# Kernel tuning notes

Measured on AMD Instinct MI355X. Metric: run time of the kernel, lower is better.

## Reference

```python
import jax, jax.numpy as jnp
import numpy as np

NHEAD = 8; DM = 512; DFF = 2048; L = 4; S = 1024; NTOK = 51; MLP = 256; CLASSES = 7
GH = 3; GHID = 64; GCLS = 5; ALPHA = 0.2
HD = DM // NHEAD

_ADJ = np.array([[0,1,0,0,0],[1,1,1,1,0],[1,0,1,0,1],[1,0,0,1,1],[0,0,1,1,1]], dtype=np.int32)


def setup_inputs():
    key = jax.random.key(0)
    ks = jax.random.split(key, 24)
    r = lambda k, s, sc=0.05: jax.random.normal(k, s, jnp.float32) * sc
    return {
        'x': jax.random.normal(ks[0], (5, S, NTOK), jnp.float32),
        'adj': jnp.asarray(_ADJ),
        'W_enc': r(ks[1], (NTOK, DM)), 'b_enc': jnp.zeros((DM,), jnp.float32),
        'cls_tok': r(ks[2], (1, 1, DM)),
        'pos_emb': r(ks[3], (S + 1, DM)),
        'Wq': r(ks[4], (L, DM, DM)), 'bq': jnp.zeros((L, DM), jnp.float32),
        'Wk': r(ks[5], (L, DM, DM)), 'bk': jnp.zeros((L, DM), jnp.float32),
        'Wv': r(ks[6], (L, DM, DM)), 'bv': jnp.zeros((L, DM), jnp.float32),
        'Wo': r(ks[7], (L, DM, DM)), 'bo': jnp.zeros((L, DM), jnp.float32),
        'W1': r(ks[8], (L, DM, DFF)), 'b1': jnp.zeros((L, DFF), jnp.float32),
        'W2': r(ks[9], (L, DFF, DM)), 'b2': jnp.zeros((L, DM), jnp.float32),
        'g1': jnp.ones((L, DM), jnp.float32), 'be1': jnp.zeros((L, DM), jnp.float32),
        'g2': jnp.ones((L, DM), jnp.float32), 'be2': jnp.zeros((L, DM), jnp.float32),
        'Wd1': r(ks[10], (DM, MLP)), 'bd1': jnp.zeros((MLP,), jnp.float32),
        'Wd2': r(ks[11], (MLP, CLASSES)), 'bd2': jnp.zeros((CLASSES,), jnp.float32),
        'Wg': r(ks[12], (GH, 3, GHID), 0.3), 'ag': r(ks[13], (GH, 2 * GHID), 0.3),
        'Wgo': r(ks[14], (GH * GHID, GCLS), 0.3), 'ago': r(ks[15], (2 * GCLS,), 0.3),
    }


def _layernorm(x, g, b, eps=1e-5):
    m = x.mean(-1, keepdims=True)
    v = ((x - m) ** 2).mean(-1, keepdims=True)
    return (x - m) * jax.lax.rsqrt(v + eps) * g + b


def _gat_attn_layer(h_in, W, a, mask):
    # standard pyGAT GraphAttentionLayer: e_ij = LeakyReLU(a1.h_i + a2.h_j)
    F = W.shape[1]
    h = h_in @ W                                                    # [N, F]
    e = jax.nn.leaky_relu((h @ a[:F])[:, None] + (h @ a[F:])[None, :], ALPHA)
    att = jax.nn.softmax(jnp.where(mask, e, -9e15), axis=-1)        # adjacency-masked softmax
    return att @ h


def _gat(xg, mask, Wg, ag, Wgo, ago):
    # xg: [5 nodes, 3 feats]; GH attention heads concatenated, then output layer
    heads = jax.vmap(lambda W, a: jax.nn.elu(_gat_attn_layer(xg, W, a, mask)))(Wg, ag)  # [GH,5,GHID]
    hcat = jnp.transpose(heads, (1, 0, 2)).reshape(xg.shape[0], GH * GHID)
    out = jax.nn.elu(_gat_attn_layer(hcat, Wgo, ago, mask))         # [5, GCLS]
    return jax.nn.log_softmax(out, axis=1)


def _forward(x, adj, params):
    (W_enc, b_enc, cls_tok, pos_emb, Wq, bq, Wk, bk, Wv, bv, Wo, bo,
     W1, b1, W2, b2, g1, be1, g2, be2, Wd1, bd1, Wd2, bd2, Wg, ag, Wgo, ago) = params
    mask = adj > 0
    # --- batched GAT: the source loops over T timesteps x 5 feature groups; here fully vectorized ---
    # x[:, :, :15] : batch(=5 nodes) x T x 15 -> [T*5groups, 5 nodes, 3]
    xg = x[:, :, :15].reshape(5, S, 5, 3)
    xg = jnp.transpose(xg, (1, 2, 0, 3)).reshape(S * 5, 5, 3)
    gat_out = jax.vmap(lambda g: _gat(g, mask, Wg, ag, Wgo, ago))(xg)
    gat_out = gat_out.reshape(S, 5, 5, GCLS)                        # [T, group, node, class]
    # --- transformer branch (eval mode: dropout = identity) ---
    h = x @ W_enc + b_enc                                           # [5, S, DM]
    h = jnp.concatenate([jnp.broadcast_to(cls_tok, (5, 1, DM)), h], axis=1)
    h = h + pos_emb[None]
    for i in range(L):
        q = (h @ Wq[i] + bq[i]).reshape(5, S + 1, NHEAD, HD)
        k = (h @ Wk[i] + bk[i]).reshape(5, S + 1, NHEAD, HD)
        v = (h @ Wv[i] + bv[i]).reshape(5, S + 1, NHEAD, HD)
        sc = jnp.einsum('bthd,bshd->bhts', q, k) / jnp.sqrt(jnp.float32(HD))
        att = jax.nn.softmax(sc, axis=-1)
        o = jnp.einsum('bhts,bshd->bthd', att, v).reshape(5, S + 1, DM) @ Wo[i] + bo[i]
        h = _layernorm(h + o, g1[i], be1[i])
        f = jax.nn.relu(h @ W1[i] + b1[i]) @ W2[i] + b2[i]
        h = _layernorm(h + f, g2[i], be2[i])
    cls = h[:, 0, :]                                                # lambda: x[:, 0, :]
    out = (cls @ Wd1 + bd1) @ Wd2 + bd2                             # no activation between dense layers (as in source)
    return out, gat_out


def reference(x, adj, W_enc, b_enc, cls_tok, pos_emb, Wq, bq, Wk, bk, Wv, bv, Wo, bo, W1, b1, W2, b2, g1, be1, g2, be2, Wd1, bd1, Wd2, bd2, Wg, ag, Wgo, ago):
    params = (W_enc, b_enc, cls_tok, pos_emb, Wq, bq, Wk, bk, Wv, bv, Wo, bo,
              W1, b1, W2, b2, g1, be1, g2, be2, Wd1, bd1, Wd2, bd2, Wg, ag, Wgo, ago)
    return _forward(x, adj, params)
```

## Files before the change

kernel.cpp:

```cpp
#include <hip/hip_runtime.h>
#include <hip/hip_bf16.h>
#include <math.h>

#define NBATCH 5
#define SEQ    1024
#define T      1025
#define ROWS   (NBATCH * T)
#define MP     5248
#define DM     512
#define DFF    2048
#define NHEAD  8
#define HD     64
#define NTOK   51
#define MLPDIM 256
#define NCLS   7
#define GH     3
#define GHID   64
#define GCLS   5
#define NGRAPH (SEQ * 5)
#define QKVN   1536
#define TPAD   1088

typedef __attribute__((ext_vector_type(8))) short bf16x8;
typedef __attribute__((ext_vector_type(4))) float f32x4;

#define GM_AS(p)  ((const __attribute__((address_space(1))) void*)(p))
#define LDS_AS(p) ((__attribute__((address_space(3))) void*)(p))

__device__ __forceinline__ unsigned short f2bf(float f) {
    unsigned int u = __float_as_uint(f);
    unsigned int r = (u + 0x7FFFu + ((u >> 16) & 1u)) >> 16;
    return (unsigned short)r;
}

__global__ __launch_bounds__(256) void wconv_kernel(
    const float* __restrict__ W, unsigned short* __restrict__ Wt, int K, int N,
    long dstride)
{
    const float* Wm = W + (size_t)blockIdx.z * K * N;
    unsigned short* Wo = Wt + (size_t)blockIdx.z * dstride;
    __shared__ float tile[32][33];
    int bx = blockIdx.x * 32;
    int by = blockIdx.y * 32;
    int tx = threadIdx.x & 31, ty = threadIdx.x >> 5;
    #pragma unroll
    for (int i = 0; i < 32; i += 8)
        tile[ty + i][tx] = Wm[(size_t)(by + ty + i) * N + bx + tx];
    __syncthreads();
    #pragma unroll
    for (int i = 0; i < 32; i += 8)
        Wo[(size_t)(bx + ty + i) * K + by + tx] = f2bf(tile[tx][ty + i]);
}

__global__ __launch_bounds__(512) void bconcat_kernel(
    const float* __restrict__ bq, const float* __restrict__ bk,
    const float* __restrict__ bv, float* __restrict__ bqkv)
{
    int i = blockIdx.x, t = threadIdx.x;
    bqkv[i * QKVN + t]        = bq[i * DM + t];
    bqkv[i * QKVN + 512 + t]  = bk[i * DM + t];
    bqkv[i * QKVN + 1024 + t] = bv[i * DM + t];
}

__global__ __launch_bounds__(256) void gemm_mfma(
    const unsigned short* __restrict__ A, const unsigned short* __restrict__ Bt,
    const float* __restrict__ bias, float* __restrict__ Cf,
    unsigned short* __restrict__ Cb, int N, int K, int relu)
{
    __shared__ unsigned short As[128 * 32];
    __shared__ unsigned short Bs[128 * 32];
    int tid = threadIdx.x;
    int l = tid & 63, w = tid >> 6;
    int wr = w & 1, wc = w >> 1;
    int mlane = l & 15, quad = l >> 4;
    int m0 = blockIdx.y * 128, n0 = blockIdx.x * 128;

    f32x4 acc[4][4] = {};

    for (int k0 = 0; k0 < K; k0 += 32) {
        __syncthreads();
        #pragma unroll
        for (int it = 0; it < 2; ++it) {
            int c = tid + it * 256;
            int row = c >> 2, cc = c & 3;
            const unsigned short* ga = A  + (size_t)(m0 + row) * K + k0 + cc * 8;
            __builtin_amdgcn_global_load_lds(GM_AS(ga), LDS_AS(As + c * 8), 16, 0, 0);
            const unsigned short* gb = Bt + (size_t)(n0 + row) * K + k0 + cc * 8;
            __builtin_amdgcn_global_load_lds(GM_AS(gb), LDS_AS(Bs + c * 8), 16, 0, 0);
        }
        __syncthreads();
        bf16x8 afrag[4], bfrag[4];
        #pragma unroll
        for (int mi = 0; mi < 4; ++mi)
            afrag[mi] = *(const bf16x8*)(As + (wr * 64 + mi * 16 + mlane) * 32 + quad * 8);
        #pragma unroll
        for (int ni = 0; ni < 4; ++ni)
            bfrag[ni] = *(const bf16x8*)(Bs + (wc * 64 + ni * 16 + mlane) * 32 + quad * 8);
        #pragma unroll
        for (int mi = 0; mi < 4; ++mi)
            #pragma unroll
            for (int ni = 0; ni < 4; ++ni)
                acc[mi][ni] = __builtin_amdgcn_mfma_f32_16x16x32_bf16(
                    afrag[mi], bfrag[ni], acc[mi][ni], 0, 0, 0);
    }

    #pragma unroll
    for (int mi = 0; mi < 4; ++mi) {
        #pragma unroll
        for (int r = 0; r < 4; ++r) {
            int gm = m0 + wr * 64 + mi * 16 + quad * 4 + r;
            size_t rowoff = (size_t)gm * N;
            #pragma unroll
            for (int ni = 0; ni < 4; ++ni) {
                int gn = n0 + wc * 64 + ni * 16 + mlane;
                float val = acc[mi][ni][r] + bias[gn];
                if (relu) val = fmaxf(val, 0.f);
                if (Cb) Cb[rowoff + gn] = f2bf(val);
                else    Cf[rowoff + gn] = val;
            }
        }
    }
}

__global__ __launch_bounds__(256) void vtrans_kernel(
    const unsigned short* __restrict__ vb, unsigned short* __restrict__ vt, int qs)
{
    __shared__ unsigned short tile[64][72];
    int bh = blockIdx.y;
    int b = bh >> 3, h = bh & 7;
    int t0 = blockIdx.x * 64;
    int tid = threadIdx.x;
    #pragma unroll
    for (int it = 0; it < 2; ++it) {
        int c = tid + it * 256;
        int key = c >> 3, cc = c & 7;
        int gk = t0 + key; if (gk >= T) gk = T - 1;
        *(bf16x8*)(&tile[key][cc * 8]) =
            *(const bf16x8*)(vb + ((size_t)b * T + gk) * qs + h * HD + cc * 8);
    }
    __syncthreads();
    #pragma unroll
    for (int it = 0; it < 2; ++it) {
        int c = tid + it * 256;
        int d = c >> 3, cc = c & 7;
        unsigned short tmp[8];
        #pragma unroll
        for (int j = 0; j < 8; ++j) tmp[j] = tile[cc * 8 + j][d];
        *(bf16x8*)(vt + ((size_t)bh * 64 + d) * TPAD + t0 + cc * 8) = *(bf16x8*)tmp;
    }
}

#define AQT 64
__global__ __launch_bounds__(256) void attn_mfma(
    const unsigned short* __restrict__ qb, const unsigned short* __restrict__ kb,
    const unsigned short* __restrict__ vt, unsigned short* __restrict__ ob,
    int qs)
{
    __shared__ unsigned short Ks[64 * 72];
    __shared__ unsigned short Vs[64 * 72];
    __shared__ unsigned short Ps[4][16 * 72];
    int bh = blockIdx.y;
    int b = bh >> 3, h = bh & 7;
    int t0 = blockIdx.x * AQT;
    int tid = threadIdx.x;
    int l = tid & 63, w = tid >> 6;
    int ml = l & 15, quad = l >> 4;
    size_t rowbase = (size_t)b * T;
    const unsigned short* vtb = vt + (size_t)bh * 64 * TPAD;

    int qrow = t0 + w * 16 + ml; if (qrow >= T) qrow = T - 1;
    const unsigned short* qp = qb + (rowbase + qrow) * qs + h * HD + quad * 8;
    bf16x8 qf0 = *(const bf16x8*)qp;
    bf16x8 qf1 = *(const bf16x8*)(qp + 32);

    f32x4 oacc[4] = {};
    float mrow[4] = {-1e30f, -1e30f, -1e30f, -1e30f};
    float lrow[4] = {0.f, 0.f, 0.f, 0.f};

    for (int c0 = 0; c0 < T; c0 += 64) {
        __syncthreads();
        #pragma unroll
        for (int it = 0; it < 2; ++it) {
            int c = tid + it * 256;
            int row = c >> 3, cc = c & 7;
            int gk = c0 + row; if (gk >= T) gk = T - 1;
            *(bf16x8*)(Ks + row * 72 + cc * 8) =
                *(const bf16x8*)(kb + (rowbase + gk) * qs + h * HD + cc * 8);
            *(bf16x8*)(Vs + row * 72 + cc * 8) =
                *(const bf16x8*)(vtb + (size_t)row * TPAD + c0 + cc * 8);
        }
        __syncthreads();

        f32x4 s[4] = {};
        #pragma unroll
        for (int ni = 0; ni < 4; ++ni) {
            bf16x8 kf0 = *(const bf16x8*)(Ks + (ni * 16 + ml) * 72 + quad * 8);
            bf16x8 kf1 = *(const bf16x8*)(Ks + (ni * 16 + ml) * 72 + 32 + quad * 8);
            s[ni] = __builtin_amdgcn_mfma_f32_16x16x32_bf16(qf0, kf0, s[ni], 0, 0, 0);
            s[ni] = __builtin_amdgcn_mfma_f32_16x16x32_bf16(qf1, kf1, s[ni], 0, 0, 0);
        }
        #pragma unroll
        for (int ni = 0; ni < 4; ++ni) {
            bool valid = (c0 + ni * 16 + ml) < T;
            #pragma unroll
            for (int r = 0; r < 4; ++r)
                s[ni][r] = valid ? s[ni][r] * 0.125f : -1e30f;
        }
        #pragma unroll
        for (int r = 0; r < 4; ++r) {
            float mx = fmaxf(fmaxf(s[0][r], s[1][r]), fmaxf(s[2][r], s[3][r]));
            #pragma unroll
            for (int off = 1; off < 16; off <<= 1)
                mx = fmaxf(mx, __shfl_xor(mx, off));
            float mnew = fmaxf(mrow[r], mx);
            float alpha = __expf(mrow[r] - mnew);
            mrow[r] = mnew;
            float rs = 0.f;
            #pragma unroll
            for (int ni = 0; ni < 4; ++ni) {
                float p = __expf(s[ni][r] - mnew);
                s[ni][r] = p; rs += p;
            }
            #pragma unroll
            for (int off = 1; off < 16; off <<= 1)
                rs += __shfl_xor(rs, off);
            lrow[r] = lrow[r] * alpha + rs;
            #pragma unroll
            for (int ni = 0; ni < 4; ++ni) oacc[ni][r] *= alpha;
        }
        unsigned short* pw = Ps[w];
        #pragma unroll
        for (int r = 0; r < 4; ++r)
            #pragma unroll
            for (int ni = 0; ni < 4; ++ni)
                pw[(quad * 4 + r) * 72 + ((ni * 16 + ml) ^ (quad << 4))] = f2bf(s[ni][r]);
        int sw = ((ml >> 2) & 3) << 4;
        #pragma unroll
        for (int kc = 0; kc < 2; ++kc) {
            bf16x8 pf = *(const bf16x8*)(pw + ml * 72 + ((kc * 32 + quad * 8) ^ sw));
            #pragma unroll
            for (int ni = 0; ni < 4; ++ni) {
                bf16x8 vf = *(const bf16x8*)(Vs + (ni * 16 + ml) * 72 + kc * 32 + quad * 8);
                oacc[ni] = __builtin_amdgcn_mfma_f32_16x16x32_bf16(pf, vf, oacc[ni], 0, 0, 0);
            }
        }
    }

    #pragma unroll
    for (int r = 0; r < 4; ++r) {
        int grow = t0 + w * 16 + quad * 4 + r;
        if (grow >= T) continue;
        float inv = 1.f / lrow[r];
        unsigned short* op = ob + (rowbase + grow) * DM + h * HD;
        #pragma unroll
        for (int ni = 0; ni < 4; ++ni)
            op[ni * 16 + ml] = f2bf(oacc[ni][r] * inv);
    }
}

__global__ __launch_bounds__(256) void encoder_kernel(
    const float* __restrict__ x, const float* __restrict__ W_enc,
    const float* __restrict__ b_enc, const float* __restrict__ cls_tok,
    const float* __restrict__ pos_emb, float* __restrict__ h,
    unsigned short* __restrict__ hb)
{
    int row = blockIdx.x;
    int b = row / T, tt = row % T;
    int tid = threadIdx.x;
    float* hp = h + (size_t)row * DM;
    unsigned short* hbp = hb + (size_t)row * DM;
    if (tt == 0) {
        float a0 = cls_tok[tid]       + pos_emb[tid];
        float a1 = cls_tok[tid + 256] + pos_emb[tid + 256];
        hp[tid] = a0; hp[tid + 256] = a1;
        hbp[tid] = f2bf(a0); hbp[tid + 256] = f2bf(a1);
        return;
    }
    __shared__ float xs[NTOK];
    int s = tt - 1;
    if (tid < NTOK) xs[tid] = x[((size_t)b * SEQ + s) * NTOK + tid];
    __syncthreads();
    #pragma unroll
    for (int rep = 0; rep < 2; ++rep) {
        int d = tid + rep * 256;
        float acc = b_enc[d] + pos_emb[(size_t)tt * DM + d];
        for (int kx = 0; kx < NTOK; ++kx) acc += xs[kx] * W_enc[kx * DM + d];
        hp[d] = acc;
        hbp[d] = f2bf(acc);
    }
}

__global__ __launch_bounds__(256) void add_ln_kernel(
    float* __restrict__ h, const float* __restrict__ r,
    const float* __restrict__ g, const float* __restrict__ be,
    unsigned short* __restrict__ hb)
{
    int w = threadIdx.x >> 6, l = threadIdx.x & 63;
    int row = blockIdx.x * 4 + w;
    if (row >= ROWS) return;
    float* hp = h + (size_t)row * DM + l * 8;
    const float* rp = r + (size_t)row * DM + l * 8;
    unsigned short* hbp = hb + (size_t)row * DM + l * 8;
    float4 a0 = *(const float4*)(hp);
    float4 a1 = *(const float4*)(hp + 4);
    float4 b0 = *(const float4*)(rp);
    float4 b1 = *(const float4*)(rp + 4);
    float v[8] = {a0.x + b0.x, a0.y + b0.y, a0.z + b0.z, a0.w + b0.w,
                  a1.x + b1.x, a1.y + b1.y, a1.z + b1.z, a1.w + b1.w};
    float s = 0.f;
    #pragma unroll
    for (int i = 0; i < 8; ++i) s += v[i];
    #pragma unroll
    for (int off = 1; off < 64; off <<= 1) s += __shfl_xor(s, off);
    float mean = s * (1.f / DM);
    float sq = 0.f;
    #pragma unroll
    for (int i = 0; i < 8; ++i) { v[i] -= mean; sq += v[i] * v[i]; }
    #pragma unroll
    for (int off = 1; off < 64; off <<= 1) sq += __shfl_xor(sq, off);
    float inv = rsqrtf(sq * (1.f / DM) + 1e-5f);
    float4 g0 = *(const float4*)(g + l * 8);
    float4 g1 = *(const float4*)(g + l * 8 + 4);
    float4 e0 = *(const float4*)(be + l * 8);
    float4 e1 = *(const float4*)(be + l * 8 + 4);
    float o[8];
    o[0] = v[0]*inv*g0.x + e0.x; o[1] = v[1]*inv*g0.y + e0.y;
    o[2] = v[2]*inv*g0.z + e0.z; o[3] = v[3]*inv*g0.w + e0.w;
    o[4] = v[4]*inv*g1.x + e1.x; o[5] = v[5]*inv*g1.y + e1.y;
    o[6] = v[6]*inv*g1.z + e1.z; o[7] = v[7]*inv*g1.w + e1.w;
    *(float4*)(hp)     = make_float4(o[0], o[1], o[2], o[3]);
    *(float4*)(hp + 4) = make_float4(o[4], o[5], o[6], o[7]);
    ushort4 p0 = {f2bf(o[0]), f2bf(o[1]), f2bf(o[2]), f2bf(o[3])};
    ushort4 p1 = {f2bf(o[4]), f2bf(o[5]), f2bf(o[6]), f2bf(o[7])};
    *(ushort4*)(hbp)     = p0;
    *(ushort4*)(hbp + 4) = p1;
}

__global__ __launch_bounds__(256) void dec1_kernel(
    const float* __restrict__ h, const float* __restrict__ Wd1,
    float* __restrict__ part)
{
    int kc = blockIdx.x, b = blockIdx.y, tid = threadIdx.x;
    __shared__ float cs[64];
    const float* cls = h + (size_t)b * T * DM;
    if (tid < 64) cs[tid] = cls[kc * 64 + tid];
    __syncthreads();
    float acc = 0.f;
    #pragma unroll
    for (int kx = 0; kx < 64; ++kx)
        acc += cs[kx] * Wd1[(size_t)(kc * 64 + kx) * MLPDIM + tid];
    part[(size_t)(b * 8 + kc) * MLPDIM + tid] = acc;
}

__global__ __launch_bounds__(256) void dec2_kernel(
    const float* __restrict__ part, const float* __restrict__ bd1,
    const float* __restrict__ Wd2, const float* __restrict__ bd2,
    float* __restrict__ out)
{
    __shared__ float t1s[MLPDIM];
    int tid = threadIdx.x;
    for (int b = 0; b < NBATCH; ++b) {
        float acc = bd1[tid];
        #pragma unroll
        for (int kc = 0; kc < 8; ++kc)
            acc += part[(size_t)(b * 8 + kc) * MLPDIM + tid];
        t1s[tid] = acc;
        __syncthreads();
        if (tid < NCLS) {
            float a2 = bd2[tid];
            for (int kx = 0; kx < MLPDIM; ++kx) a2 += t1s[kx] * Wd2[kx * NCLS + tid];
            out[b * NCLS + tid] = a2;
        }
        __syncthreads();
    }
}

__global__ __launch_bounds__(64) void gat_kernel(
    const float* __restrict__ x, const int* __restrict__ adj,
    const float* __restrict__ Wg, const float* __restrict__ ag,
    const float* __restrict__ Wgo, const float* __restrict__ ago,
    float* __restrict__ out)
{
    int g = blockIdx.x;
    int s = g / 5, jj = g % 5;
    int tid = threadIdx.x;
    __shared__ float xs[5][3];
    __shared__ int adjs[25];
    __shared__ float hb[GH][5][GHID];
    __shared__ float o1[GH][5][GHID];
    __shared__ float srcb[GH][5], dstb[GH][5];
    __shared__ float attb[GH][5][5];
    __shared__ float h2[5][5], src2[5], dst2[5], att2[5][5], o2[5][5];

    if (tid < 15) { int n = tid / 3, c = tid % 3;
        xs[n][c] = x[(size_t)n * SEQ * NTOK + (size_t)s * NTOK + jj * 3 + c]; }
    if (tid < 25) adjs[tid] = adj[tid];
    __syncthreads();

    #pragma unroll
    for (int hh = 0; hh < GH; ++hh)
        #pragma unroll
        for (int n = 0; n < 5; ++n)
            hb[hh][n][tid] = xs[n][0] * Wg[hh * 192 + tid]
                           + xs[n][1] * Wg[hh * 192 + 64 + tid]
                           + xs[n][2] * Wg[hh * 192 + 128 + tid];
    __syncthreads();

    if (tid < 15) { int hh = tid / 5, n = tid % 5; float a = 0.f;
        for (int f = 0; f < GHID; ++f) a += hb[hh][n][f] * ag[hh * 128 + f];
        srcb[hh][n] = a;
    } else if (tid >= 32 && tid < 47) { int t2 = tid - 32; int hh = t2 / 5, n = t2 % 5; float a = 0.f;
        for (int f = 0; f < GHID; ++f) a += hb[hh][n][f] * ag[hh * 128 + 64 + f];
        dstb[hh][n] = a;
    }
    __syncthreads();

    if (tid < 15) { int hh = tid / 5, i = tid % 5;
        float e[5]; float mx = -1e30f;
        #pragma unroll
        for (int j2 = 0; j2 < 5; ++j2) {
            float ev = srcb[hh][i] + dstb[hh][j2];
            ev = ev > 0.f ? ev : 0.2f * ev;
            e[j2] = ev;
            if (adjs[i * 5 + j2] && ev > mx) mx = ev;
        }
        float sum = 0.f;
        #pragma unroll
        for (int j2 = 0; j2 < 5; ++j2) {
            float p = adjs[i * 5 + j2] ? expf(e[j2] - mx) : 0.f;
            e[j2] = p; sum += p;
        }
        float inv = 1.f / sum;
        #pragma unroll
        for (int j2 = 0; j2 < 5; ++j2) attb[hh][i][j2] = e[j2] * inv;
    }
    __syncthreads();

    #pragma unroll
    for (int hh = 0; hh < GH; ++hh)
        #pragma unroll
        for (int n = 0; n < 5; ++n) {
            float a = 0.f;
            #pragma unroll
            for (int j2 = 0; j2 < 5; ++j2) a += attb[hh][n][j2] * hb[hh][j2][tid];
            o1[hh][n][tid] = a > 0.f ? a : expm1f(a);
        }
    __syncthreads();

    if (tid < 25) { int n = tid / 5, m = tid % 5; float a = 0.f;
        for (int hh = 0; hh < GH; ++hh)
            for (int f = 0; f < GHID; ++f)
                a += o1[hh][n][f] * Wgo[(hh * GHID + f) * GCLS + m];
        h2[n][m] = a;
    }
    __syncthreads();

    if (tid < 5) { float a = 0.f;
        for (int m = 0; m < GCLS; ++m) a += h2[tid][m] * ago[m];
        src2[tid] = a;
    } else if (tid >= 8 && tid < 13) { int n = tid - 8; float a = 0.f;
        for (int m = 0; m < GCLS; ++m) a += h2[n][m] * ago[GCLS + m];
        dst2[n] = a;
    }
    __syncthreads();

    if (tid < 5) { int i = tid;
        float e[5]; float mx = -1e30f;
        #pragma unroll
        for (int j2 = 0; j2 < 5; ++j2) {
            float ev = src2[i] + dst2[j2];
            ev = ev > 0.f ? ev : 0.2f * ev;
            e[j2] = ev;
            if (adjs[i * 5 + j2] && ev > mx) mx = ev;
        }
        float sum = 0.f;
        #pragma unroll
        for (int j2 = 0; j2 < 5; ++j2) {
            float p = adjs[i * 5 + j2] ? expf(e[j2] - mx) : 0.f;
            e[j2] = p; sum += p;
        }
        float inv = 1.f / sum;
        #pragma unroll
        for (int j2 = 0; j2 < 5; ++j2) att2[i][j2] = e[j2] * inv;
    }
    __syncthreads();

    if (tid < 25) { int n = tid / 5, m = tid % 5; float a = 0.f;
        #pragma unroll
        for (int j2 = 0; j2 < 5; ++j2) a += att2[n][j2] * h2[j2][m];
        o2[n][m] = a > 0.f ? a : expm1f(a);
    }
    __syncthreads();

    if (tid < 5) { int n = tid;
        float mx = o2[n][0];
        #pragma unroll
        for (int m = 1; m < GCLS; ++m) mx = fmaxf(mx, o2[n][m]);
        float sum = 0.f;
        #pragma unroll
        for (int m = 0; m < GCLS; ++m) sum += expf(o2[n][m] - mx);
        float ls = logf(sum);
        #pragma unroll
        for (int m = 0; m < GCLS; ++m)
            out[(size_t)g * 25 + n * 5 + m] = o2[n][m] - mx - ls;
    }
}

extern "C" void kernel_launch(void* const* d_in, const int* in_sizes, int n_in,
                              void* d_out, int out_size, void* d_ws, size_t ws_size,
                              hipStream_t stream)
{
    const float* x       = (const float*)d_in[0];
    const int*   adj     = (const int*)  d_in[1];
    const float* W_enc   = (const float*)d_in[2];
    const float* b_enc   = (const float*)d_in[3];
    const float* cls_tok = (const float*)d_in[4];
    const float* pos_emb = (const float*)d_in[5];
    const float* Wq = (const float*)d_in[6];
    const float* bq = (const float*)d_in[7];
    const float* Wk = (const float*)d_in[8];
    const float* bk = (const float*)d_in[9];
    const float* Wv = (const float*)d_in[10];
    const float* bv = (const float*)d_in[11];
    const float* Wo = (const float*)d_in[12];
    const float* bo = (const float*)d_in[13];
    const float* W1 = (const float*)d_in[14];
    const float* b1 = (const float*)d_in[15];
    const float* W2 = (const float*)d_in[16];
    const float* b2 = (const float*)d_in[17];
    const float* g1 = (const float*)d_in[18];
    const float* be1= (const float*)d_in[19];
    const float* g2 = (const float*)d_in[20];
    const float* be2= (const float*)d_in[21];
    const float* Wd1= (const float*)d_in[22];
    const float* bd1= (const float*)d_in[23];
    const float* Wd2= (const float*)d_in[24];
    const float* bd2= (const float*)d_in[25];
    const float* Wg = (const float*)d_in[26];
    const float* ag = (const float*)d_in[27];
    const float* Wgo= (const float*)d_in[28];
    const float* ago= (const float*)d_in[29];
    float* out = (float*)d_out;

    float* ws = (float*)d_ws;
    float* h = ws;
    float* q = h + (size_t)MP * DM;
    unsigned short* hb   = (unsigned short*)(q + (size_t)MP * DM);
    unsigned short* qkvb = hb + (size_t)MP * DM;
    unsigned short* ob   = qkvb + (size_t)MP * QKVN;
    unsigned short* f1b  = qkvb;
    unsigned short* Wqkvt= ob + (size_t)MP * DM;
    unsigned short* Wot  = Wqkvt + (size_t)4 * QKVN * DM;
    unsigned short* W1t  = Wot + (size_t)4 * DM * DM;
    unsigned short* W2t  = W1t + (size_t)4 * DM * DFF;
    float* bqkv = (float*)(W2t + (size_t)4 * DFF * DM);
    float* dpart = bqkv + 4 * QKVN;
    unsigned short* vt = (unsigned short*)(dpart + NBATCH * 8 * MLPDIM);

    const long QS = (long)QKVN * DM;
    wconv_kernel<<<dim3(DM/32,  DM/32,  4), 256, 0, stream>>>(Wq, Wqkvt,            DM,  DM, QS);
    wconv_kernel<<<dim3(DM/32,  DM/32,  4), 256, 0, stream>>>(Wk, Wqkvt + 512*512,  DM,  DM, QS);
    wconv_kernel<<<dim3(DM/32,  DM/32,  4), 256, 0, stream>>>(Wv, Wqkvt + 1024*512, DM,  DM, QS);
    wconv_kernel<<<dim3(DM/32,  DM/32,  4), 256, 0, stream>>>(Wo, Wot, DM,  DM, (long)DM*DM);
    wconv_kernel<<<dim3(DFF/32, DM/32,  4), 256, 0, stream>>>(W1, W1t, DM,  DFF, (long)DM*DFF);
    wconv_kernel<<<dim3(DM/32,  DFF/32, 4), 256, 0, stream>>>(W2, W2t, DFF, DM, (long)DFF*DM);
    bconcat_kernel<<<4, 512, 0, stream>>>(bq, bk, bv, bqkv);

    gat_kernel<<<NGRAPH, 64, 0, stream>>>(x, adj, Wg, ag, Wgo, ago, out + NBATCH * NCLS);
    encoder_kernel<<<ROWS, 256, 0, stream>>>(x, W_enc, b_enc, cls_tok, pos_emb, h, hb);

    dim3 g512 (DM  / 128, MP / 128);
    dim3 gqkv (QKVN / 128, MP / 128);
    dim3 g2048(DFF / 128, MP / 128);
    dim3 gAttn(TPAD / AQT, NBATCH * NHEAD);
    dim3 gVt  (TPAD / 64, NBATCH * NHEAD);
    int gLN = (ROWS + 3) / 4;

    for (int i = 0; i < 4; ++i) {
        gemm_mfma<<<gqkv, 256, 0, stream>>>(hb, Wqkvt + (size_t)i*QKVN*DM, bqkv + i*QKVN, nullptr, qkvb, QKVN, DM, 0);
        vtrans_kernel<<<gVt, 256, 0, stream>>>(qkvb + 1024, vt, QKVN);
        attn_mfma<<<gAttn, 256, 0, stream>>>(qkvb, qkvb + 512, vt, ob, QKVN);
        gemm_mfma<<<g512, 256, 0, stream>>>(ob, Wot + (size_t)i*DM*DM, bo + i*DM, q, nullptr, DM, DM, 0);
        add_ln_kernel<<<gLN, 256, 0, stream>>>(h, q, g1 + i*DM, be1 + i*DM, hb);
        gemm_mfma<<<g2048, 256, 0, stream>>>(hb,  W1t + (size_t)i*DM*DFF, b1 + i*DFF, nullptr, f1b, DFF, DM, 1);
        gemm_mfma<<<g512, 256, 0, stream>>>(f1b, W2t + (size_t)i*DM*DFF, b2 + i*DM,  q, nullptr, DM, DFF, 0);
        add_ln_kernel<<<gLN, 256, 0, stream>>>(h, q, g2 + i*DM, be2 + i*DM, hb);
    }

    dec1_kernel<<<dim3(8, NBATCH), 256, 0, stream>>>(h, Wd1, dpart);
    dec2_kernel<<<1, 256, 0, stream>>>(dpart, bd1, Wd2, bd2, out);
}
```

Measured before the change: 959.1 us.

## Double K-step in GEMM and register-prefetch next K/V chunk in attention

The bf16 MFMA GEMM now stages a 64-wide K slice per iteration instead of 32. That halves the number of barrier and load rounds per tile, at the cost of twice the LDS. The attention kernel now loads the next K/V chunk into registers while computing on the current one, so global memory latency overlaps the MFMA work. Both changes raise register and LDS pressure, which may reduce occupancy.

```diff
diff --git a/kernel.cpp b/kernel.cpp
--- a/kernel.cpp
+++ b/kernel.cpp
@@ -67,8 +67,8 @@
     const float* __restrict__ bias, float* __restrict__ Cf,
     unsigned short* __restrict__ Cb, int N, int K, int relu)
 {
-    __shared__ unsigned short As[128 * 32];
-    __shared__ unsigned short Bs[128 * 32];
+    __shared__ unsigned short As[128 * 64];
+    __shared__ unsigned short Bs[128 * 64];
     int tid = threadIdx.x;
     int l = tid & 63, w = tid >> 6;
     int wr = w & 1, wc = w >> 1;
@@ -77,31 +77,35 @@
 
     f32x4 acc[4][4] = {};
 
-    for (int k0 = 0; k0 < K; k0 += 32) {
+    for (int k0 = 0; k0 < K; k0 += 64) {
         __syncthreads();
         #pragma unroll
-        for (int it = 0; it < 2; ++it) {
+        for (int it = 0; it < 4; ++it) {
             int c = tid + it * 256;
-            int row = c >> 2, cc = c & 3;
+            int row = c >> 3, cc = c & 7;
             const unsigned short* ga = A  + (size_t)(m0 + row) * K + k0 + cc * 8;
             __builtin_amdgcn_global_load_lds(GM_AS(ga), LDS_AS(As + c * 8), 16, 0, 0);
             const unsigned short* gb = Bt + (size_t)(n0 + row) * K + k0 + cc * 8;
             __builtin_amdgcn_global_load_lds(GM_AS(gb), LDS_AS(Bs + c * 8), 16, 0, 0);
         }
         __syncthreads();
-        bf16x8 afrag[4], bfrag[4];
-        #pragma unroll
-        for (int mi = 0; mi < 4; ++mi)
-            afrag[mi] = *(const bf16x8*)(As + (wr * 64 + mi * 16 + mlane) * 32 + quad * 8);
-        #pragma unroll
-        for (int ni = 0; ni < 4; ++ni)
-            bfrag[ni] = *(const bf16x8*)(Bs + (wc * 64 + ni * 16 + mlane) * 32 + quad * 8);
-        #pragma unroll
-        for (int mi = 0; mi < 4; ++mi)
+        #pragma unroll
+        for (int half = 0; half < 2; ++half) {
+            int ko = half * 32 + quad * 8;
+            bf16x8 afrag[4], bfrag[4];
+            #pragma unroll
+            for (int mi = 0; mi < 4; ++mi)
+                afrag[mi] = *(const bf16x8*)(As + (wr * 64 + mi * 16 + mlane) * 64 + ko);
             #pragma unroll
             for (int ni = 0; ni < 4; ++ni)
-                acc[mi][ni] = __builtin_amdgcn_mfma_f32_16x16x32_bf16(
-                    afrag[mi], bfrag[ni], acc[mi][ni], 0, 0, 0);
+                bfrag[ni] = *(const bf16x8*)(Bs + (wc * 64 + ni * 16 + mlane) * 64 + ko);
+            #pragma unroll
+            for (int mi = 0; mi < 4; ++mi)
+                #pragma unroll
+                for (int ni = 0; ni < 4; ++ni)
+                    acc[mi][ni] = __builtin_amdgcn_mfma_f32_16x16x32_bf16(
+                        afrag[mi], bfrag[ni], acc[mi][ni], 0, 0, 0);
+        }
     }
 
     #pragma unroll
@@ -151,6 +155,7 @@
 }
 
 #define AQT 64
+#define NCH 17
 __global__ __launch_bounds__(256) void attn_mfma(
     const unsigned short* __restrict__ qb, const unsigned short* __restrict__ kb,
     const unsigned short* __restrict__ vt, unsigned short* __restrict__ ob,
@@ -173,23 +178,40 @@
     bf16x8 qf0 = *(const bf16x8*)qp;
     bf16x8 qf1 = *(const bf16x8*)(qp + 32);
 
+    int c_a = tid, c_b = tid + 256;
+    int rowa = c_a >> 3, cca = c_a & 7;
+    int rowb = c_b >> 3, ccb = c_b & 7;
+
     f32x4 oacc[4] = {};
     float mrow[4] = {-1e30f, -1e30f, -1e30f, -1e30f};
     float lrow[4] = {0.f, 0.f, 0.f, 0.f};
 
-    for (int c0 = 0; c0 < T; c0 += 64) {
+    bf16x8 kra, krb, vra, vrb;
+    {
+        int gka = rowa;  int gkb = rowb;
+        kra = *(const bf16x8*)(kb + (rowbase + gka) * qs + h * HD + cca * 8);
+        krb = *(const bf16x8*)(kb + (rowbase + gkb) * qs + h * HD + ccb * 8);
+        vra = *(const bf16x8*)(vtb + (size_t)rowa * TPAD + 0 + cca * 8);
+        vrb = *(const bf16x8*)(vtb + (size_t)rowb * TPAD + 0 + ccb * 8);
+    }
+
+    for (int ch = 0; ch < NCH; ++ch) {
+        int c0 = ch * 64;
         __syncthreads();
-        #pragma unroll
-        for (int it = 0; it < 2; ++it) {
-            int c = tid + it * 256;
-            int row = c >> 3, cc = c & 7;
-            int gk = c0 + row; if (gk >= T) gk = T - 1;
-            *(bf16x8*)(Ks + row * 72 + cc * 8) =
-                *(const bf16x8*)(kb + (rowbase + gk) * qs + h * HD + cc * 8);
-            *(bf16x8*)(Vs + row * 72 + cc * 8) =
-                *(const bf16x8*)(vtb + (size_t)row * TPAD + c0 + cc * 8);
-        }
+        *(bf16x8*)(Ks + rowa * 72 + cca * 8) = kra;
+        *(bf16x8*)(Ks + rowb * 72 + ccb * 8) = krb;
+        *(bf16x8*)(Vs + rowa * 72 + cca * 8) = vra;
+        *(bf16x8*)(Vs + rowb * 72 + ccb * 8) = vrb;
         __syncthreads();
+        if (ch + 1 < NCH) {
+            int n0k = c0 + 64;
+            int gka = n0k + rowa; if (gka >= T) gka = T - 1;
+            int gkb = n0k + rowb; if (gkb >= T) gkb = T - 1;
+            kra = *(const bf16x8*)(kb + (rowbase + gka) * qs + h * HD + cca * 8);
+            krb = *(const bf16x8*)(kb + (rowbase + gkb) * qs + h * HD + ccb * 8);
+            vra = *(const bf16x8*)(vtb + (size_t)rowa * TPAD + n0k + cca * 8);
+            vrb = *(const bf16x8*)(vtb + (size_t)rowb * TPAD + n0k + ccb * 8);
+        }
 
         f32x4 s[4] = {};
         #pragma unroll
```

Measured after the change: 957.7 us. No clear change (-0.1%).
